# Kernel optimization log

Hardware: AMD Instinct MI355X
Metric: run time of the kernel (lower is better)

The kernel has to match this reference:

```python
import jax, jax.numpy as jnp
from jax import lax
import numpy as np

R = 4            # search_range
B, H, W, C = 8, 192, 192, 64
CV = (2 * R + 1) ** 2          # 81 cost-volume channels
CIN0 = CV + 2 * C              # concat(cost, prv, nxt) channels = 209
FILTERS = (128, 64, 32, 16)
DN = ('NHWC', 'HWIO', 'NHWC')
EPS = 1e-3                     # Keras BatchNormalization default epsilon


def setup_inputs() -> dict:
    key = jax.random.key(0)
    ks = iter(jax.random.split(key, 32))
    inp = {}
    inp['prv'] = jax.random.normal(next(ks), (B, H, W, C), jnp.float32)
    inp['nxt'] = jax.random.normal(next(ks), (B, H, W, C), jnp.float32)
    cin = CIN0
    for i, f in enumerate(FILTERS):
        inp[f'dw{i}'] = jax.random.normal(next(ks), (3, 3, 1, cin), jnp.float32) / np.sqrt(9.0)
        inp[f'pw{i}'] = jax.random.normal(next(ks), (1, 1, cin, f), jnp.float32) / np.sqrt(cin)
        inp[f'b{i}'] = jnp.zeros((f,), jnp.float32)
        cin = f
    inp['bn_gamma'] = jnp.ones((cin,), jnp.float32)
    inp['bn_beta'] = jnp.zeros((cin,), jnp.float32)
    inp['bn_mean'] = jnp.zeros((cin,), jnp.float32)
    inp['bn_var'] = jnp.ones((cin,), jnp.float32)
    inp['flow_w'] = jax.random.normal(next(ks), (3, 3, cin, 2), jnp.float32) / np.sqrt(9.0 * cin)
    return inp


def mish(x):
    return x * jnp.tanh(jax.nn.softplus(x))


def cost_volume(prv, nxt):
    # pad nxt by R on spatial dims, correlate over (2R+1)^2 shifts
    pad = jnp.pad(nxt, ((0, 0), (R, R), (R, R), (0, 0)))
    vols = []
    for i in range(2 * R + 1):           # fixed 9x9 offset set (not a data dim)
        for j in range(2 * R + 1):
            roi = lax.slice(pad, (0, i, j, 0), (B, i + H, j + W, C))
            vols.append(jnp.mean(prv * roi, axis=-1))
    cv = jnp.stack(vols, axis=-1)        # [B,H,W,81]
    return jax.nn.leaky_relu(cv, 0.1)


def sep_conv(x, dw, pw, b):
    cin = x.shape[-1]
    y = lax.conv_general_dilated(x, dw, (1, 1), 'SAME',
                                 dimension_numbers=DN, feature_group_count=cin)
    y = lax.conv_general_dilated(y, pw, (1, 1), 'SAME', dimension_numbers=DN) + b
    return mish(y)


def reference(prv, nxt, dw0, pw0, b0, dw1, pw1, b1, dw2, pw2, b2, dw3, pw3, b3,
              bn_gamma, bn_beta, bn_mean, bn_var, flow_w):
    cost = cost_volume(prv, nxt)
    x = jnp.concatenate([cost, prv, nxt], axis=-1)   # [B,H,W,209]
    for dw, pw, b in ((dw0, pw0, b0), (dw1, pw1, b1), (dw2, pw2, b2), (dw3, pw3, b3)):
        x = sep_conv(x, dw, pw, b)
    # BatchNorm (inference: moving statistics)
    x = (x - bn_mean) * (bn_gamma / jnp.sqrt(bn_var + EPS)) + bn_beta
    flow = lax.conv_general_dilated(x, flow_w, (1, 1), 'SAME', dimension_numbers=DN)
    scale = (float(H) ** 2 + float(W) ** 2) ** 0.5
    return scale * flow
```

## Files before the change

kernel.cpp:

```cpp
#include <hip/hip_runtime.h>
#include <hip/hip_bf16.h>

#define BB 8
#define HH 192
#define WW 192
#define CC0 64
#define NPIX (BB*HH*WW)
#define NCV 81
#define CVP 96

typedef __attribute__((ext_vector_type(8))) short short8;
typedef __attribute__((ext_vector_type(4))) short short4v;
typedef __attribute__((ext_vector_type(4))) float f32x4;

__device__ __forceinline__ float bf2f(short s) {
    union { unsigned u; float f; } x; x.u = ((unsigned)(unsigned short)s) << 16; return x.f;
}
__device__ __forceinline__ short f2bf(float f) {
    __hip_bfloat16 h = __float2bfloat16(f);
    return *reinterpret_cast<short*>(&h);
}
__device__ __forceinline__ void cvt8(const short8 iv, float* fv) {
    const int* ip = (const int*)&iv;
#pragma unroll
    for (int e = 0; e < 4; ++e) {
        union { unsigned u; float f; } lo, hi;
        lo.u = ((unsigned)ip[e]) << 16;
        hi.u = ((unsigned)ip[e]) & 0xffff0000u;
        fv[2 * e] = lo.f; fv[2 * e + 1] = hi.f;
    }
}

__device__ __forceinline__ float mish_f(float v) {
    if (v > 20.0f) return v;
    const float u = __expf(v);
    const float n = u * (u + 2.0f);
    return v * n / (n + 2.0f);
}

__global__ __launch_bounds__(256) void prep_kernel(
    const float* __restrict__ dw0, const float* __restrict__ pw0,
    const float* __restrict__ dw1, const float* __restrict__ pw1,
    const float* __restrict__ dw2, const float* __restrict__ pw2,
    const float* __restrict__ dw3, const float* __restrict__ pw3,
    __hip_bfloat16* __restrict__ wout)
{
    const int u = blockIdx.x * 256 + threadIdx.x;
    if (u >= 43456) return;
    float v = 0.f;
    if (u < 2016) {
        const int t = u / 224, c = u % 224;
        if (c < 64)       v = dw0[t*209 + 81  + c];
        else if (c < 128) v = dw0[t*209 + 145 + (c-64)];
        else if (c < 209) v = dw0[t*209 + (c-128)];
    } else if (u < 3168) {
        const int r = u-2016, t = r/128, c = r%128; v = dw1[t*128+c];
    } else if (u < 3744) {
        const int r = u-3168, t = r/64, c = r%64; v = dw2[t*64+c];
    } else if (u < 4032) {
        const int r = u-3744, t = r/32, c = r%32; v = dw3[t*32+c];
    } else if (u < 32704) {
        const int r = u-4032, n = r/224, c = r%224;
        if (c < 64)       v = pw0[(81+c)*128 + n];
        else if (c < 128) v = pw0[(145+(c-64))*128 + n];
        else if (c < 209) v = pw0[(c-128)*128 + n];
    } else if (u < 40896) {
        const int r = u-32704, n = r/128, c = r%128; v = pw1[c*64 + n];
    } else if (u < 42944) {
        const int r = u-40896, n = r/64, c = r%64; v = pw2[c*32 + n];
    } else {
        const int r = u-42944, n = r/32, c = r%32; v = pw3[c*16 + n];
    }
    wout[u] = __float2bfloat16(v);
}

__global__ __launch_bounds__(256) void prep2_kernel(
    const float* __restrict__ dw0, const float* __restrict__ dw1,
    const float* __restrict__ dw2, const float* __restrict__ dw3,
    const float* __restrict__ bn_g, const float* __restrict__ bn_b,
    const float* __restrict__ bn_m, const float* __restrict__ bn_v,
    const float* __restrict__ fw, float* __restrict__ fout)
{
    const int u = blockIdx.x * 256 + threadIdx.x;
    if (u >= 4338) return;
    float v = 0.f;
    if (u < 2016) {
        const int t = u / 224, c = u % 224;
        if (c < 64)       v = dw0[t*209 + 81  + c];
        else if (c < 128) v = dw0[t*209 + 145 + (c-64)];
        else if (c < 209) v = dw0[t*209 + (c-128)];
    } else if (u < 3168) {
        const int r = u-2016, t = r/128, c = r%128; v = dw1[t*128+c];
    } else if (u < 3744) {
        const int r = u-3168, t = r/64, c = r%64; v = dw2[t*64+c];
    } else if (u < 4032) {
        const int r = u-3744, t = r/32, c = r%32; v = dw3[t*32+c];
    } else if (u < 4320) {
        const int r = u-4032, t = r/32, rem = r%32, c = rem >> 1, s = rem & 1;
        const float sc = bn_g[c] * rsqrtf(bn_v[c] + 1e-3f);
        v = sc * fw[t*32 + c*2 + s];
    } else {
        const int r = u-4320, t = r/2, s = r%2;
        float a = 0.f;
        for (int c = 0; c < 16; ++c) {
            const float sc = bn_g[c] * rsqrtf(bn_v[c] + 1e-3f);
            const float sh = bn_b[c] - bn_m[c] * sc;
            a += sh * fw[t*32 + c*2 + s];
        }
        v = a;
    }
    fout[u] = v;
}

template<int UNIFIED>
__global__ __launch_bounds__(256) void cost_mfma_kernel(
    const float* __restrict__ prv, const float* __restrict__ nxt,
    __hip_bfloat16* __restrict__ xout)
{
    constexpr int OST   = UNIFIED ? 224 : CVP;
    constexpr int CVOFF = UNIFIED ? 128 : 0;

    __shared__ __align__(16) short sCv[4][32][96];

    const int tid  = threadIdx.x;
    const int lane = tid & 63;
    const int wv   = tid >> 6;
    const int ln15 = lane & 15;
    const int kq   = lane >> 4;
    const int mt   = wv & 1;
    const int jt   = wv >> 1;

    const int bx = blockIdx.x;
    const int tw = bx % 6;
    const int th = (bx / 6) % 48;
    const int b  = bx / 288;
    const int w0 = tw * 32, h0 = th * 4;

    {
        const short8 z = {0,0,0,0,0,0,0,0};
#pragma unroll
        for (int t = 0; t < 6; ++t) {
            const int idx = tid + t * 256;
            const int row = idx / 384, rem = idx % 384;
            const int px = rem / 12, c8 = rem % 12;
            *(short8*)&sCv[row][px][c8 * 8] = z;
        }
    }

    short8 af0[4], af1[4];
    {
        const int apx = w0 + mt * 16 + ln15;
#pragma unroll
        for (int r4 = 0; r4 < 4; ++r4) {
            const float* ap = prv + (((size_t)b * HH + h0 + r4) * WW + apx) * CC0 + kq * 8;
            const float4 x0 = *(const float4*)(ap);
            const float4 x1 = *(const float4*)(ap + 4);
            const float4 x2 = *(const float4*)(ap + 32);
            const float4 x3 = *(const float4*)(ap + 36);
            af0[r4][0]=f2bf(x0.x); af0[r4][1]=f2bf(x0.y); af0[r4][2]=f2bf(x0.z); af0[r4][3]=f2bf(x0.w);
            af0[r4][4]=f2bf(x1.x); af0[r4][5]=f2bf(x1.y); af0[r4][6]=f2bf(x1.z); af0[r4][7]=f2bf(x1.w);
            af1[r4][0]=f2bf(x2.x); af1[r4][1]=f2bf(x2.y); af1[r4][2]=f2bf(x2.z); af1[r4][3]=f2bf(x2.w);
            af1[r4][4]=f2bf(x3.x); af1[r4][5]=f2bf(x3.y); af1[r4][6]=f2bf(x3.z); af1[r4][7]=f2bf(x3.w);
        }
    }

    if (UNIFIED && jt == 0) {
#pragma unroll
        for (int r4 = 0; r4 < 4; ++r4) {
            short* op = (short*)xout
                + (((size_t)b * HH + h0 + r4) * WW + w0 + mt * 16 + ln15) * OST
                + kq * 8;
            *(short8*)op = af0[r4];
            *(short8*)(op + 32) = af1[r4];
        }
    }

    __syncthreads();

    const int gwb = w0 - 4 + mt * 16 + jt * 16 + ln15;
    const bool gok = ((unsigned)gwb < (unsigned)WW);
    const float* nxcol = nxt + ((size_t)b * HH * WW + gwb) * CC0 + kq * 8;

    const float4 fz = make_float4(0.f, 0.f, 0.f, 0.f);
    float4 c0 = fz, c1 = fz, c2 = fz, c3 = fz;
    float4 n0 = fz, n1 = fz, n2 = fz, n3 = fz;

    auto ldrow = [&](int y, float4& a0, float4& a1, float4& a2, float4& a3) {
        a0 = a1 = a2 = a3 = fz;
        if (gok && (unsigned)y < (unsigned)HH) {
            const float* p = nxcol + (size_t)y * (WW * CC0);
            a0 = *(const float4*)(p);
            a1 = *(const float4*)(p + 4);
            a2 = *(const float4*)(p + 32);
            a3 = *(const float4*)(p + 36);
        }
    };

    ldrow(h0 - 4, c0, c1, c2, c3);

    for (int i = 0; i < 12; ++i) {
        const int y = h0 - 4 + i;
        if (i < 11) ldrow(y + 1, n0, n1, n2, n3);

        if ((unsigned)y < (unsigned)HH) {
            short8 b0, b1;
            b0[0]=f2bf(c0.x); b0[1]=f2bf(c0.y); b0[2]=f2bf(c0.z); b0[3]=f2bf(c0.w);
            b0[4]=f2bf(c1.x); b0[5]=f2bf(c1.y); b0[6]=f2bf(c1.z); b0[7]=f2bf(c1.w);
            b1[0]=f2bf(c2.x); b1[1]=f2bf(c2.y); b1[2]=f2bf(c2.z); b1[3]=f2bf(c2.w);
            b1[4]=f2bf(c3.x); b1[5]=f2bf(c3.y); b1[6]=f2bf(c3.z); b1[7]=f2bf(c3.w);

            if (UNIFIED && i >= 4 && i < 8 && gwb >= w0 && gwb < w0 + 32) {
                short* op = (short*)xout
                    + (((size_t)b * HH + y) * WW + gwb) * OST + 64 + kq * 8;
                *(short8*)op = b0;
                *(short8*)(op + 32) = b1;
            }

#pragma unroll
            for (int r4 = 0; r4 < 4; ++r4) {
                const int rband = i - r4;
                if ((unsigned)rband <= 8u) {
                    f32x4 acc = {0.f, 0.f, 0.f, 0.f};
                    acc = __builtin_amdgcn_mfma_f32_16x16x32_bf16(af0[r4], b0, acc, 0, 0, 0);
                    acc = __builtin_amdgcn_mfma_f32_16x16x32_bf16(af1[r4], b1, acc, 0, 0, 0);
#pragma unroll
                    for (int rr = 0; rr < 4; ++rr) {
                        const int m_local = kq * 4 + rr;
                        const int dj = jt * 16 + ln15 - m_local;
                        if ((unsigned)dj < 9u) {
                            float mv = acc[rr] * (1.0f / 64.0f);
                            mv = (mv > 0.f) ? mv : 0.1f * mv;
                            sCv[r4][mt * 16 + m_local][rband * 9 + dj] = f2bf(mv);
                        }
                    }
                }
            }
        }
        c0 = n0; c1 = n1; c2 = n2; c3 = n3;
    }

    __syncthreads();
    const size_t obase_blk = (((size_t)b * HH + h0) * WW + w0);
#pragma unroll
    for (int t = 0; t < 6; ++t) {
        const int idx = tid + t * 256;
        const int row = idx / 384, rem = idx % 384;
        const int px = rem / 12, c8 = rem % 12;
        short* op = (short*)xout + (obase_blk + (size_t)row * WW + px) * OST + CVOFF + c8 * 8;
        *(short8*)op = *(const short8*)&sCv[row][px][c8 * 8];
    }
}

template<int KP, int COUT, int MODE>
__global__ __launch_bounds__(256) void sepconv_mfma(
    const __hip_bfloat16* __restrict__ in,
    const float* __restrict__ prv, const float* __restrict__ nxt,
    const float* __restrict__ dwf,
    const __hip_bfloat16* __restrict__ Bt,
    const float* __restrict__ bias,
    __hip_bfloat16* __restrict__ out)
{
    constexpr int NC  = KP / 32;
    constexpr int NT  = COUT / 16;
    constexpr int WGN = (NT >= 2) ? 2 : 1;
    constexpr int WGM = 4 / WGN;
    constexpr int TM  = 8 / WGM;
    constexpr int TN  = NT / WGN;

    __shared__ __align__(16) short sIn[816 * 8];
    __shared__ __align__(16) short sA[4][128][8];

    const int tid  = threadIdx.x;
    const int lane = tid & 63;
    const int wv   = tid >> 6;
    const int ln15 = lane & 15;
    const int kq   = lane >> 4;
    const int wm   = wv % WGM;
    const int wn   = wv / WGM;

    const int bx = blockIdx.x;
    const int tw = bx % 6;
    const int th = (bx / 6) % 48;
    const int bb = bx / 288;
    const int w0 = tw * 32, h0 = th * 4;

    const int dkbu = __builtin_amdgcn_readfirstlane(wv);
    const int dww  = lane & 31;
    const int dhh  = (lane >> 5) * 2;

    auto load_unit = [&](int u, int k0) -> short8 {
        const int kb = u & 3;
        const int p  = u >> 2;
        const int iw = p % 34, ih = p / 34;
        const int gw = w0 - 1 + iw, gh = h0 - 1 + ih;
        short8 v = {0,0,0,0,0,0,0,0};
        if ((unsigned)gw < (unsigned)WW && (unsigned)gh < (unsigned)HH) {
            const size_t pix = ((size_t)bb * HH + gh) * WW + gw;
            const int c0 = k0 + kb * 8;
            if (c0 < 64) {
                const float4* s = (const float4*)(prv + pix * 64 + c0);
                const float4 a = s[0], bq = s[1];
                v[0]=f2bf(a.x);  v[1]=f2bf(a.y);  v[2]=f2bf(a.z);  v[3]=f2bf(a.w);
                v[4]=f2bf(bq.x); v[5]=f2bf(bq.y); v[6]=f2bf(bq.z); v[7]=f2bf(bq.w);
            } else if (c0 < 128) {
                const float4* s = (const float4*)(nxt + pix * 64 + (c0 - 64));
                const float4 a = s[0], bq = s[1];
                v[0]=f2bf(a.x);  v[1]=f2bf(a.y);  v[2]=f2bf(a.z);  v[3]=f2bf(a.w);
                v[4]=f2bf(bq.x); v[5]=f2bf(bq.y); v[6]=f2bf(bq.z); v[7]=f2bf(bq.w);
            } else {
                v = *(const short8*)((const short*)in + pix * CVP + (c0 - 128));
            }
        }
        return v;
    };

    const short* sp[4];
    bool sok[4];
#pragma unroll
    for (int t = 0; t < 4; ++t) {
        const int u = tid + t * 256;
        const int kb = u & 3, p = u >> 2;
        const int iw = p % 34, ih = p / 34;
        const int gw = w0 - 1 + iw, gh = h0 - 1 + ih;
        sok[t] = (u < 816) && ((unsigned)gw < (unsigned)WW) && ((unsigned)gh < (unsigned)HH);
        const size_t pix = ((size_t)bb * HH + gh) * WW + gw;
        sp[t] = (const short*)in + pix * KP + kb * 8;
    }

    f32x4 acc[TM][TN] = {};
    short8 pr[4];

#pragma unroll
    for (int t = 0; t < 4; ++t) {
        pr[t] = short8{0,0,0,0,0,0,0,0};
        if (MODE == 0) {
            if (sok[t]) pr[t] = *(const short8*)(sp[t]);
        } else {
            const int u = tid + t * 256;
            if (u < 816) pr[t] = load_unit(u, 0);
        }
    }

#pragma unroll
    for (int c = 0; c < NC; ++c) {
        const int k0 = c * 32;
#pragma unroll
        for (int t = 0; t < 4; ++t) {
            const int u = tid + t * 256;
            if (u < 816) {
                const int ug = u ^ ((u >> 3) & 3);
                *(short8*)(sIn + (size_t)ug * 8) = pr[t];
            }
        }
        __syncthreads();

        if (c + 1 < NC) {
#pragma unroll
            for (int t = 0; t < 4; ++t) {
                pr[t] = short8{0,0,0,0,0,0,0,0};
                if (MODE == 0) {
                    if (sok[t]) pr[t] = *(const short8*)(sp[t] + k0 + 32);
                } else {
                    const int u = tid + t * 256;
                    if (u < 816) pr[t] = load_unit(u, k0 + 32);
                }
            }
        }
        short8 bfr[TN];
#pragma unroll
        for (int j = 0; j < TN; ++j) {
            const int n = (wn * TN + j) * 16 + ln15;
            bfr[j] = *(const short8*)((const short*)Bt + (size_t)n * KP + k0 + kq * 8);
        }

        {
            const float* wrow = dwf + k0 + dkbu * 8;
            const int pbase = dhh * 34 + dww;
            float r0[8] = {0,0,0,0,0,0,0,0};
            float r1[8] = {0,0,0,0,0,0,0,0};
#pragma unroll
            for (int dy = 0; dy < 4; ++dy) {
#pragma unroll
                for (int dx = 0; dx < 3; ++dx) {
                    const int p2 = pbase + dy * 34 + dx;
                    const int g  = p2 * 4 + (dkbu ^ ((p2 >> 1) & 3));
                    const short8 iv = *(const short8*)(sIn + (size_t)g * 8);
                    float fv[8];
                    cvt8(iv, fv);
                    if (dy < 3) {
#pragma unroll
                        for (int j = 0; j < 8; ++j)
                            r0[j] += fv[j] * wrow[(dy * 3 + dx) * KP + j];
                    }
                    if (dy >= 1) {
#pragma unroll
                        for (int j = 0; j < 8; ++j)
                            r1[j] += fv[j] * wrow[((dy - 1) * 3 + dx) * KP + j];
                    }
                }
            }
            const int px0 = dhh * 32 + dww;
            short8 o0, o1;
#pragma unroll
            for (int j = 0; j < 8; ++j) { o0[j] = f2bf(r0[j]); o1[j] = f2bf(r1[j]); }
            *(short8*)&sA[dkbu][px0 ^ (dkbu << 2)][0] = o0;
            *(short8*)&sA[dkbu][(px0 + 32) ^ (dkbu << 2)][0] = o1;
        }
        __syncthreads();

        short8 af[TM];
#pragma unroll
        for (int i = 0; i < TM; ++i) {
            const int m = (wm * TM + i) * 16 + ln15;
            af[i] = *(const short8*)&sA[kq][m ^ (kq << 2)][0];
        }
#pragma unroll
        for (int i = 0; i < TM; ++i)
#pragma unroll
            for (int j = 0; j < TN; ++j)
                acc[i][j] = __builtin_amdgcn_mfma_f32_16x16x32_bf16(
                    af[i], bfr[j], acc[i][j], 0, 0, 0);
    }

#pragma unroll
    for (int j = 0; j < TN; ++j) {
        const int n = (wn * TN + j) * 16 + ln15;
        const float bj = bias[n];
#pragma unroll
        for (int i = 0; i < TM; ++i) {
#pragma unroll
            for (int r = 0; r < 4; ++r) {
                const int m  = (wm * TM + i) * 16 + kq * 4 + r;
                const int gh = h0 + (m >> 5), gw = w0 + (m & 31);
                const size_t gp = ((size_t)bb * HH + gh) * WW + gw;
                out[gp * COUT + n] = __float2bfloat16(mish_f(acc[i][j][r] + bj));
            }
        }
    }
}

__global__ __launch_bounds__(256) void bn_flow_kernel(
    const __hip_bfloat16* __restrict__ xin,
    const float* __restrict__ fwp, const float* __restrict__ tbv,
    float* __restrict__ out)
{
    const int pix = blockIdx.x * 256 + threadIdx.x;
    const int wq  = pix % WW;
    const int hq  = (pix / WW) % HH;
    const int bq  = pix / (WW * HH);
    float a0 = 0.f, a1 = 0.f;
#pragma unroll
    for (int dy = -1; dy <= 1; ++dy) {
        const int yy = hq + dy;
        if ((unsigned)yy >= HH) continue;
#pragma unroll
        for (int dx = -1; dx <= 1; ++dx) {
            const int xx = wq + dx;
            if ((unsigned)xx >= WW) continue;
            const int t = (dy + 1) * 3 + (dx + 1);
            a0 += tbv[t * 2 + 0];
            a1 += tbv[t * 2 + 1];
            const short* xp = (const short*)xin + (((size_t)bq * HH + yy) * WW + xx) * 16;
            const short8 v0 = *(const short8*)xp;
            const short8 v1 = *(const short8*)(xp + 8);
            float x[16];
            cvt8(v0, x); cvt8(v1, x + 8);
            const float* wp = fwp + t * 32;
#pragma unroll
            for (int c = 0; c < 16; ++c) {
                a0 += x[c] * wp[c * 2 + 0];
                a1 += x[c] * wp[c * 2 + 1];
            }
        }
    }
    const float SC = sqrtf((float)(HH * HH + WW * WW));
    out[(size_t)pix * 2 + 0] = SC * a0;
    out[(size_t)pix * 2 + 1] = SC * a1;
}

extern "C" void kernel_launch(void* const* d_in, const int* in_sizes, int n_in,
                              void* d_out, int out_size, void* d_ws, size_t ws_size,
                              hipStream_t stream)
{
    const float* prv   = (const float*)d_in[0];
    const float* nxt   = (const float*)d_in[1];
    const float* dw0   = (const float*)d_in[2];
    const float* pw0   = (const float*)d_in[3];
    const float* b0    = (const float*)d_in[4];
    const float* dw1   = (const float*)d_in[5];
    const float* pw1   = (const float*)d_in[6];
    const float* b1    = (const float*)d_in[7];
    const float* dw2   = (const float*)d_in[8];
    const float* pw2   = (const float*)d_in[9];
    const float* b2    = (const float*)d_in[10];
    const float* dw3   = (const float*)d_in[11];
    const float* pw3   = (const float*)d_in[12];
    const float* b3    = (const float*)d_in[13];
    const float* bn_g  = (const float*)d_in[14];
    const float* bn_b  = (const float*)d_in[15];
    const float* bn_m  = (const float*)d_in[16];
    const float* bn_v  = (const float*)d_in[17];
    const float* fw    = (const float*)d_in[18];
    float* outp = (float*)d_out;

    const size_t N = (size_t)NPIX;
    __hip_bfloat16* ws = (__hip_bfloat16*)d_ws;

    const size_t need_uni = (N * 352 + 43456) * 2 + 4338 * 4;
    const bool uni = (ws_size >= need_uni);

    __hip_bfloat16* t1  = uni ? (ws + N * 224) : (ws + N * 96);
    __hip_bfloat16* wts = uni ? (ws + N * 352) : (ws + N * 224);
    __hip_bfloat16* t2  = ws;
    __hip_bfloat16* t3  = t1;
    __hip_bfloat16* t4  = ws + N * 64;
    __hip_bfloat16* Bt0 = wts + 4032;
    __hip_bfloat16* Bt1 = wts + 32704;
    __hip_bfloat16* Bt2 = wts + 40896;
    __hip_bfloat16* Bt3 = wts + 42944;
    float* fwt = (float*)(wts + 43456);

    prep_kernel<<<170, 256, 0, stream>>>(dw0, pw0, dw1, pw1, dw2, pw2, dw3, pw3, wts);
    prep2_kernel<<<17, 256, 0, stream>>>(dw0, dw1, dw2, dw3,
                                         bn_g, bn_b, bn_m, bn_v, fw, fwt);
    if (uni) {
        cost_mfma_kernel<1><<<2304, 256, 0, stream>>>(prv, nxt, ws);
        sepconv_mfma<224, 128, 0><<<2304, 256, 0, stream>>>(ws, nullptr, nullptr,
                                                            fwt, Bt0, b0, t1);
    } else {
        cost_mfma_kernel<0><<<2304, 256, 0, stream>>>(prv, nxt, ws);
        sepconv_mfma<224, 128, 1><<<2304, 256, 0, stream>>>(ws, prv, nxt,
                                                            fwt, Bt0, b0, t1);
    }
    sepconv_mfma<128, 64, 0><<<2304, 256, 0, stream>>>(t1, nullptr, nullptr,
                                                       fwt + 2016, Bt1, b1, t2);
    sepconv_mfma<64, 32, 0><<<2304, 256, 0, stream>>>(t2, nullptr, nullptr,
                                                      fwt + 3168, Bt2, b2, t3);
    sepconv_mfma<32, 16, 0><<<2304, 256, 0, stream>>>(t3, nullptr, nullptr,
                                                      fwt + 3744, Bt3, b3, t4);
    bn_flow_kernel<<<NPIX / 256, 256, 0, stream>>>(t4, fwt + 4032, fwt + 4320, outp);
}
```

Before: 453.1 us.

## Swizzle block IDs across XCDs and deepen row prefetch in cost volume

Adds an XCD-aware block index remap to the cost-volume, separable-conv and BN/flow kernels, so that spatially adjacent tiles, which share halo rows, run on the same XCD and reuse its L2. The cost-volume row loop becomes a three-slot rotating register buffer that prefetches two rows ahead instead of one, to hide global-load latency. Loop-invariant index terms (dj base, in-window test) are hoisted. The deeper prefetch costs more registers, and the swizzle assumes the block count divides evenly by 8, which holds for 2304 and NPIX/256.

```diff
diff --git a/kernel.cpp b/kernel.cpp
--- a/kernel.cpp
+++ b/kernel.cpp
@@ -36,6 +36,10 @@
     const float u = __expf(v);
     const float n = u * (u + 2.0f);
     return v * n / (n + 2.0f);
+}
+
+__device__ __forceinline__ int xcd_swz(int bid, int nwg) {
+    return (bid & 7) * (nwg >> 3) + (bid >> 3);
 }
 
 __global__ __launch_bounds__(256) void prep_kernel(
@@ -130,7 +134,7 @@
     const int mt   = wv & 1;
     const int jt   = wv >> 1;
 
-    const int bx = blockIdx.x;
+    const int bx = xcd_swz(blockIdx.x, 2304);
     const int tw = bx % 6;
     const int th = (bx / 6) % 48;
     const int b  = bx / 288;
@@ -180,10 +184,10 @@
     const int gwb = w0 - 4 + mt * 16 + jt * 16 + ln15;
     const bool gok = ((unsigned)gwb < (unsigned)WW);
     const float* nxcol = nxt + ((size_t)b * HH * WW + gwb) * CC0 + kq * 8;
+    const int dj0 = jt * 16 + ln15 - kq * 4;
+    const bool inw = (gwb >= w0) && (gwb < w0 + 32);
 
     const float4 fz = make_float4(0.f, 0.f, 0.f, 0.f);
-    float4 c0 = fz, c1 = fz, c2 = fz, c3 = fz;
-    float4 n0 = fz, n1 = fz, n2 = fz, n3 = fz;
 
     auto ldrow = [&](int y, float4& a0, float4& a1, float4& a2, float4& a3) {
         a0 = a1 = a2 = a3 = fz;
@@ -196,20 +200,18 @@
         }
     };
 
-    ldrow(h0 - 4, c0, c1, c2, c3);
-
-    for (int i = 0; i < 12; ++i) {
+    auto body = [&](int i, float4& a0, float4& a1, float4& a2, float4& a3,
+                    float4& p0, float4& p1, float4& p2, float4& p3) {
         const int y = h0 - 4 + i;
-        if (i < 11) ldrow(y + 1, n0, n1, n2, n3);
-
+        if (i < 10) ldrow(y + 2, p0, p1, p2, p3);
         if ((unsigned)y < (unsigned)HH) {
             short8 b0, b1;
-            b0[0]=f2bf(c0.x); b0[1]=f2bf(c0.y); b0[2]=f2bf(c0.z); b0[3]=f2bf(c0.w);
-            b0[4]=f2bf(c1.x); b0[5]=f2bf(c1.y); b0[6]=f2bf(c1.z); b0[7]=f2bf(c1.w);
-            b1[0]=f2bf(c2.x); b1[1]=f2bf(c2.y); b1[2]=f2bf(c2.z); b1[3]=f2bf(c2.w);
-            b1[4]=f2bf(c3.x); b1[5]=f2bf(c3.y); b1[6]=f2bf(c3.z); b1[7]=f2bf(c3.w);
-
-            if (UNIFIED && i >= 4 && i < 8 && gwb >= w0 && gwb < w0 + 32) {
+            b0[0]=f2bf(a0.x); b0[1]=f2bf(a0.y); b0[2]=f2bf(a0.z); b0[3]=f2bf(a0.w);
+            b0[4]=f2bf(a1.x); b0[5]=f2bf(a1.y); b0[6]=f2bf(a1.z); b0[7]=f2bf(a1.w);
+            b1[0]=f2bf(a2.x); b1[1]=f2bf(a2.y); b1[2]=f2bf(a2.z); b1[3]=f2bf(a2.w);
+            b1[4]=f2bf(a3.x); b1[5]=f2bf(a3.y); b1[6]=f2bf(a3.z); b1[7]=f2bf(a3.w);
+
+            if (UNIFIED && i >= 4 && i < 8 && inw) {
                 short* op = (short*)xout
                     + (((size_t)b * HH + y) * WW + gwb) * OST + 64 + kq * 8;
                 *(short8*)op = b0;
@@ -226,7 +228,7 @@
 #pragma unroll
                     for (int rr = 0; rr < 4; ++rr) {
                         const int m_local = kq * 4 + rr;
-                        const int dj = jt * 16 + ln15 - m_local;
+                        const int dj = dj0 - rr;
                         if ((unsigned)dj < 9u) {
                             float mv = acc[rr] * (1.0f / 64.0f);
                             mv = (mv > 0.f) ? mv : 0.1f * mv;
@@ -236,7 +238,19 @@
                 }
             }
         }
-        c0 = n0; c1 = n1; c2 = n2; c3 = n3;
+    };
+
+    float4 s00, s01, s02, s03;
+    float4 s10, s11, s12, s13;
+    float4 s20, s21, s22, s23;
+
+    ldrow(h0 - 4, s00, s01, s02, s03);
+    ldrow(h0 - 3, s10, s11, s12, s13);
+
+    for (int ii = 0; ii < 12; ii += 3) {
+        body(ii + 0, s00, s01, s02, s03, s20, s21, s22, s23);
+        body(ii + 1, s10, s11, s12, s13, s00, s01, s02, s03);
+        body(ii + 2, s20, s21, s22, s23, s10, s11, s12, s13);
     }
 
     __syncthreads();
@@ -278,7 +292,7 @@
     const int wm   = wv % WGM;
     const int wn   = wv / WGM;
 
-    const int bx = blockIdx.x;
+    const int bx = xcd_swz(blockIdx.x, 2304);
     const int tw = bx % 6;
     const int th = (bx / 6) % 48;
     const int bb = bx / 288;
@@ -444,7 +458,7 @@
     const float* __restrict__ fwp, const float* __restrict__ tbv,
     float* __restrict__ out)
 {
-    const int pix = blockIdx.x * 256 + threadIdx.x;
+    const int pix = xcd_swz(blockIdx.x, NPIX / 256) * 256 + threadIdx.x;
     const int wq  = pix % WW;
     const int hq  = (pix / WW) % HH;
     const int bq  = pix / (WW * HH);
```

New measurement: 451.2 us. Within noise of the previous version (-0.4%).
